# Performance work log

Measured on AMD Instinct MI355X. Metric: run time of the kernel, lower is better.

## Reference

```python
import jax, jax.numpy as jnp
import numpy as np

NUM_BINS = 256
EPS = 1e-8


def setup_inputs() -> dict:
    key = jax.random.key(0)
    k1, k2 = jax.random.split(key)
    x = jax.random.uniform(k1, (4096, 8192), dtype=jnp.float32)
    y = jax.random.uniform(k2, (4096, 8192), dtype=jnp.float32)
    return {"x": x, "y": y}


def reference(x, y):
    # min-max normalize to [0, 1]
    xn = (x - jnp.min(x)) / (jnp.max(x) - jnp.min(x) + EPS)
    yn = (y - jnp.min(y)) / (jnp.max(y) - jnp.min(y) + EPS)
    # bin indices, clamped to [0, NUM_BINS-1] (floor(1.0*N) == N gets clipped)
    x_idx = jnp.clip(jnp.floor(xn * NUM_BINS).astype(jnp.int32), 0, NUM_BINS - 1)
    y_idx = jnp.clip(jnp.floor(yn * NUM_BINS).astype(jnp.int32), 0, NUM_BINS - 1)
    n = x.shape[0] * x.shape[1]
    # joint histogram via scatter-add on flattened (x_idx, y_idx) pairs
    flat = (x_idx * NUM_BINS + y_idx).reshape(-1)
    hist_xy = jnp.zeros((NUM_BINS * NUM_BINS,), jnp.float32).at[flat].add(1.0)
    hist_xy = hist_xy.reshape(NUM_BINS, NUM_BINS)
    p_xy = hist_xy / n
    p_x = jnp.sum(p_xy, axis=1)  # marginal over y
    p_y = jnp.sum(p_xy, axis=0)  # marginal over x
    # MI: sum over cells where p_xy>0 and both marginals>0
    px_py = p_x[:, None] * p_y[None, :]
    valid = (p_xy > 0) & (p_x[:, None] > 0) & (p_y[None, :] > 0)
    safe_pxy = jnp.where(valid, p_xy, 1.0)
    safe_den = jnp.where(valid, px_py, 1.0)
    mi = jnp.sum(jnp.where(valid, p_xy * jnp.log(safe_pxy / safe_den), 0.0))
    # normalized MI
    h_x = -jnp.sum(p_x * jnp.log(p_x + EPS))
    h_y = -jnp.sum(p_y * jnp.log(p_y + EPS))
    mi = mi / (jnp.sqrt(h_x * h_y) + EPS)
    return -mi
```

## Files before the change

kernel.cpp:

```cpp
#include <hip/hip_runtime.h>
#include <stdint.h>
#include <math.h>

#define HIST_BINS   65536
#define HIST_WORDS8 16384
#define NTHR_HIST   1024

__device__ __forceinline__ uint32_t f2key(float f){
    uint32_t u = __float_as_uint(f);
    return (u & 0x80000000u) ? ~u : (u | 0x80000000u);
}
__device__ __forceinline__ float key2f(uint32_t k){
    uint32_t u = (k & 0x80000000u) ? (k ^ 0x80000000u) : ~k;
    return __uint_as_float(u);
}


__global__ void init_mm_kernel(uint32_t* __restrict__ mm){
    mm[0] = 0xFFFFFFFFu;
    mm[1] = 0u;
    mm[2] = 0xFFFFFFFFu;
    mm[3] = 0u;
}

__device__ __forceinline__ void mm4(float4 a, float& mn, float& mx){
    mn = fminf(mn, fminf(fminf(a.x, a.y), fminf(a.z, a.w)));
    mx = fmaxf(mx, fmaxf(fmaxf(a.x, a.y), fmaxf(a.z, a.w)));
}

__global__ void __launch_bounds__(1024)
minmax_kernel(const float4* __restrict__ x, const float4* __restrict__ y,
              uint32_t* __restrict__ mm, int n4, int nblk_per){
    int isy = (blockIdx.x >= (unsigned)nblk_per) ? 1 : 0;
    const float4* __restrict__ src = isy ? y : x;
    int bid = blockIdx.x - isy * nblk_per;
    float mn = INFINITY, mx = -INFINITY;
    int stride = nblk_per * blockDim.x;
    int i = bid * blockDim.x + threadIdx.x;
    for (; i + 7 * stride < n4; i += 8 * stride){
        float4 v0 = src[i];
        float4 v1 = src[i +     stride];
        float4 v2 = src[i + 2 * stride];
        float4 v3 = src[i + 3 * stride];
        float4 v4 = src[i + 4 * stride];
        float4 v5 = src[i + 5 * stride];
        float4 v6 = src[i + 6 * stride];
        float4 v7 = src[i + 7 * stride];
        mm4(v0, mn, mx); mm4(v1, mn, mx); mm4(v2, mn, mx); mm4(v3, mn, mx);
        mm4(v4, mn, mx); mm4(v5, mn, mx); mm4(v6, mn, mx); mm4(v7, mn, mx);
    }
    for (; i < n4; i += stride) mm4(src[i], mn, mx);

    #pragma unroll
    for (int off = 32; off > 0; off >>= 1){
        mn = fminf(mn, __shfl_down(mn, off, 64));
        mx = fmaxf(mx, __shfl_down(mx, off, 64));
    }
    __shared__ float smn[16], smx[16];
    int lane = threadIdx.x & 63, wid = threadIdx.x >> 6;
    if (lane == 0){ smn[wid] = mn; smx[wid] = mx; }
    __syncthreads();
    if (threadIdx.x == 0){
        int nw = blockDim.x >> 6;
        for (int w = 1; w < nw; ++w){
            mn = fminf(mn, smn[w]); mx = fmaxf(mx, smx[w]);
        }
        atomicMin(&mm[isy * 2 + 0], f2key(mn));
        atomicMax(&mm[isy * 2 + 1], f2key(mx));
    }
}

__device__ __forceinline__ void bin_pair(float vx, float vy,
                                         float mnx, float sx, float mny, float sy,
                                         uint32_t* lh){
    int ix = (int)floorf((vx - mnx) * sx);
    int iy = (int)floorf((vy - mny) * sy);
    ix = ix < 0 ? 0 : (ix > 255 ? 255 : ix);
    iy = iy < 0 ? 0 : (iy > 255 ? 255 : iy);
    uint32_t bin = ((uint32_t)ix << 8) | (uint32_t)iy;
    atomicAdd(&lh[bin >> 2], 1u << ((bin & 3u) * 8u));
}

__device__ __forceinline__ void bin4(float4 a, float4 b,
                                     float mnx, float sx, float mny, float sy,
                                     uint32_t* lh){
    bin_pair(a.x, b.x, mnx, sx, mny, sy, lh);
    bin_pair(a.y, b.y, mnx, sx, mny, sy, lh);
    bin_pair(a.z, b.z, mnx, sx, mny, sy, lh);
    bin_pair(a.w, b.w, mnx, sx, mny, sy, lh);
}

__global__ void __launch_bounds__(NTHR_HIST)
hist_kernel(const float4* __restrict__ x, const float4* __restrict__ y,
            const uint32_t* __restrict__ mm, uint32_t* __restrict__ out32,
            int n4, int atomic_flush){
    __shared__ uint32_t lh[HIST_WORDS8];
    for (int w = threadIdx.x; w < HIST_WORDS8; w += blockDim.x) lh[w] = 0u;
    __syncthreads();

    float mnx = key2f(mm[0]);
    float sx  = 256.0f / ((key2f(mm[1]) - mnx) + 1e-8f);
    float mny = key2f(mm[2]);
    float sy  = 256.0f / ((key2f(mm[3]) - mny) + 1e-8f);

    int stride = gridDim.x * blockDim.x;
    int i = blockIdx.x * blockDim.x + threadIdx.x;
    for (; i + 3 * stride < n4; i += 4 * stride){
        float4 a0 = x[i], a1 = x[i + stride], a2 = x[i + 2*stride], a3 = x[i + 3*stride];
        float4 b0 = y[i], b1 = y[i + stride], b2 = y[i + 2*stride], b3 = y[i + 3*stride];
        bin4(a0, b0, mnx, sx, mny, sy, lh);
        bin4(a1, b1, mnx, sx, mny, sy, lh);
        bin4(a2, b2, mnx, sx, mny, sy, lh);
        bin4(a3, b3, mnx, sx, mny, sy, lh);
    }
    for (; i < n4; i += stride){
        float4 a = x[i], b = y[i];
        bin4(a, b, mnx, sx, mny, sy, lh);
    }
    __syncthreads();

    if (!atomic_flush){
        uint32_t* part = out32 + (size_t)blockIdx.x * HIST_WORDS8;
        for (int w = threadIdx.x; w < HIST_WORDS8; w += blockDim.x) part[w] = lh[w];
    } else {
        for (int w = threadIdx.x; w < HIST_WORDS8; w += blockDim.x){
            uint32_t v = lh[w];
            if (v){
                uint32_t c0 = v & 255u, c1 = (v >> 8) & 255u, c2 = (v >> 16) & 255u, c3 = v >> 24;
                if (c0) atomicAdd(&out32[4*w + 0], c0);
                if (c1) atomicAdd(&out32[4*w + 1], c1);
                if (c2) atomicAdd(&out32[4*w + 2], c2);
                if (c3) atomicAdd(&out32[4*w + 3], c3);
            }
        }
    }
}

__global__ void __launch_bounds__(1024)
reduce_kernel(const uint32_t* __restrict__ partials, uint32_t* __restrict__ hist,
              int nparts){
    __shared__ uint32_t sm[64][16][16];
    int t = threadIdx.x;
    int ql = t & 15, g = t >> 4;
    int per = nparts >> 6;
    uint32_t c[16];
    #pragma unroll
    for (int k = 0; k < 16; ++k) c[k] = 0;
    const uint4* base = (const uint4*)partials;
    size_t qoff = (size_t)blockIdx.x * 16 + ql;
    #pragma unroll 8
    for (int j = 0; j < per; ++j){
        uint4 v = base[(size_t)(g * per + j) * (HIST_WORDS8 / 4) + qoff];
        c[ 0] += v.x & 255u; c[ 1] += (v.x >> 8) & 255u; c[ 2] += (v.x >> 16) & 255u; c[ 3] += v.x >> 24;
        c[ 4] += v.y & 255u; c[ 5] += (v.y >> 8) & 255u; c[ 6] += (v.y >> 16) & 255u; c[ 7] += v.y >> 24;
        c[ 8] += v.z & 255u; c[ 9] += (v.z >> 8) & 255u; c[10] += (v.z >> 16) & 255u; c[11] += v.z >> 24;
        c[12] += v.w & 255u; c[13] += (v.w >> 8) & 255u; c[14] += (v.w >> 16) & 255u; c[15] += v.w >> 24;
    }
    #pragma unroll
    for (int k = 0; k < 16; ++k) sm[g][k][ql] = c[k];
    __syncthreads();
    if (t < 256){
        int q2 = t & 15;
        int k  = t >> 4;
        uint32_t s = 0;
        #pragma unroll 8
        for (int gg = 0; gg < 64; ++gg) s += sm[gg][k][q2];
        hist[((size_t)blockIdx.x * 16 + q2) * 16 + k] = s;
    }
}

__device__ double bsum1024(double v, double* red, int t){
    #pragma unroll
    for (int off = 32; off > 0; off >>= 1) v += __shfl_down(v, off, 64);
    __syncthreads();
    if ((t & 63) == 0) red[t >> 6] = v;
    __syncthreads();
    if (t == 0){
        double s = 0.0;
        for (int w = 0; w < 16; ++w) s += red[w];
        v = s;
    }
    return v;
}

__global__ void __launch_bounds__(1024)
finalize_kernel(const uint32_t* __restrict__ hist, float* __restrict__ out, int n){
    __shared__ uint32_t rsum[256];
    __shared__ uint32_t csum4[4][256];
    __shared__ uint32_t csum[256];
    __shared__ double red[16];
    int t = threadIdx.x;

    {
        int r = t >> 2, q = t & 3;
        const uint4* hp = (const uint4*)(hist + r * 256 + q * 64);
        uint32_t s = 0;
        #pragma unroll
        for (int k = 0; k < 16; ++k){
            uint4 v = hp[k];
            s += v.x + v.y + v.z + v.w;
        }
        s += __shfl_down(s, 2, 64);
        s += __shfl_down(s, 1, 64);
        if (q == 0) rsum[r] = s;
    }
    {
        int c = t & 255, g = t >> 8;
        const uint32_t* hp = hist + g * 64 * 256 + c;
        uint32_t s = 0;
        #pragma unroll 8
        for (int r = 0; r < 64; ++r) s += hp[r * 256];
        csum4[g][c] = s;
    }
    __syncthreads();
    if (t < 256) csum[t] = csum4[0][t] + csum4[1][t] + csum4[2][t] + csum4[3][t];
    __syncthreads();

    const double invn = 1.0 / (double)n;
    const double dn = (double)n;

    double mi = 0.0;
    {
        int c = t & 255, rb = t >> 8;
        double cs = (double)csum[c];
        for (int k = 0; k < 64; ++k){
            int r = k * 4 + rb;
            uint32_t cnt = hist[r * 256 + c];
            if (cnt){
                double rs = (double)rsum[r];
                double ratio = ((double)cnt * dn) / (rs * cs);
                mi += (double)cnt * (double)logf((float)ratio);
            }
        }
        mi *= invn;
    }
    double hx = 0.0, hy = 0.0;
    if (t < 256){
        double px = (double)rsum[t] * invn;
        double py = (double)csum[t] * invn;
        hx = px * log(px + 1e-8);
        hy = py * log(py + 1e-8);
    }
    double mi_s = bsum1024(mi, red, t);
    double hx_s = bsum1024(hx, red, t);
    double hy_s = bsum1024(hy, red, t);
    if (t == 0){
        double h_x = -hx_s, h_y = -hy_s;
        double nmi = mi_s / (sqrt(h_x * h_y) + 1e-8);
        out[0] = (float)(-nmi);
    }
}

extern "C" void kernel_launch(void* const* d_in, const int* in_sizes, int n_in,
                              void* d_out, int out_size, void* d_ws, size_t ws_size,
                              hipStream_t stream){
    const float* x = (const float*)d_in[0];
    const float* y = (const float*)d_in[1];
    float* out = (float*)d_out;
    uint32_t* ws = (uint32_t*)d_ws;
    uint32_t* hist = ws;
    uint32_t* mm = ws + HIST_BINS;
    uint32_t* partials = ws + HIST_BINS + 64;

    int n  = in_sizes[0];
    int n4 = n / 4;

    size_t need512 = ((size_t)HIST_BINS + 64 + (size_t)512 * HIST_WORDS8) * 4;
    size_t need256 = ((size_t)HIST_BINS + 64 + (size_t)256 * HIST_WORDS8) * 4;
    int nblk, atomic_flush;
    if (ws_size >= need512)      { nblk = 512; atomic_flush = 0; }
    else if (ws_size >= need256) { nblk = 256; atomic_flush = 0; }
    else                         { nblk = 512; atomic_flush = 1; }

    if (atomic_flush)
        hipMemsetAsync(hist, 0, HIST_BINS * sizeof(uint32_t), stream);
    init_mm_kernel<<<1, 1, 0, stream>>>(mm);
    minmax_kernel<<<512, 1024, 0, stream>>>((const float4*)x, (const float4*)y, mm, n4, 256);
    hist_kernel<<<nblk, NTHR_HIST, 0, stream>>>((const float4*)x, (const float4*)y, mm,
                                                atomic_flush ? hist : partials, n4, atomic_flush);
    if (!atomic_flush)
        reduce_kernel<<<256, 1024, 0, stream>>>(partials, hist, nblk);
    finalize_kernel<<<1, 1024, 0, stream>>>(hist, out, n);
}
```

Before: 367.9 us.

## Use contiguous per-block segments, nontemporal loads, and fuse marginals into reduce

Minmax and histogram kernels now have each block walk its own contiguous segment instead of a grid-stride pattern, and the histogram kernel reads inputs with nontemporal loads. The reduce kernel now also computes row sums and column sums of the joint histogram, using atomics for the column sums. Finalize can then skip recomputing the marginals and reads the histogram in a vectorized row-major order. The goal is better DRAM locality and less serial work in the single-block finalize, at the cost of extra atomics and an init kernel that clears the column-sum buffer.

```diff
diff --git a/kernel.cpp b/kernel.cpp
--- a/kernel.cpp
+++ b/kernel.cpp
@@ -4,7 +4,10 @@
 
 #define HIST_BINS   65536
 #define HIST_WORDS8 16384
-#define NTHR_HIST   1024
+
+typedef float f4 __attribute__((ext_vector_type(4)));
+
+__device__ __forceinline__ f4 ldnt(const f4* p){ return __builtin_nontemporal_load(p); }
 
 __device__ __forceinline__ uint32_t f2key(float f){
     uint32_t u = __float_as_uint(f);
@@ -16,55 +19,50 @@
 }
 
 
-__global__ void init_mm_kernel(uint32_t* __restrict__ mm){
-    mm[0] = 0xFFFFFFFFu;
-    mm[1] = 0u;
-    mm[2] = 0xFFFFFFFFu;
-    mm[3] = 0u;
-}
-
-__device__ __forceinline__ void mm4(float4 a, float& mn, float& mx){
-    mn = fminf(mn, fminf(fminf(a.x, a.y), fminf(a.z, a.w)));
-    mx = fmaxf(mx, fmaxf(fmaxf(a.x, a.y), fmaxf(a.z, a.w)));
+__global__ void init_kernel(uint32_t* __restrict__ mm, uint32_t* __restrict__ csum){
+    int t = threadIdx.x;
+    if (t < 4) mm[t] = (t & 1) ? 0u : 0xFFFFFFFFu;
+    csum[t] = 0u;
+}
+
+__device__ __forceinline__ void mm4(f4 a, float& mn, float& mx){
+    mn = fminf(mn, fminf(fminf(a[0], a[1]), fminf(a[2], a[3])));
+    mx = fmaxf(mx, fmaxf(fmaxf(a[0], a[1]), fmaxf(a[2], a[3])));
 }
 
 __global__ void __launch_bounds__(1024)
-minmax_kernel(const float4* __restrict__ x, const float4* __restrict__ y,
+minmax_kernel(const f4* __restrict__ x, const f4* __restrict__ y,
               uint32_t* __restrict__ mm, int n4, int nblk_per){
     int isy = (blockIdx.x >= (unsigned)nblk_per) ? 1 : 0;
-    const float4* __restrict__ src = isy ? y : x;
+    const f4* __restrict__ src = isy ? y : x;
     int bid = blockIdx.x - isy * nblk_per;
+    int seg = n4 / nblk_per;
+    int base = bid * seg;
+    const int chunk = 1024 * 8;
     float mn = INFINITY, mx = -INFINITY;
-    int stride = nblk_per * blockDim.x;
-    int i = bid * blockDim.x + threadIdx.x;
-    for (; i + 7 * stride < n4; i += 8 * stride){
-        float4 v0 = src[i];
-        float4 v1 = src[i +     stride];
-        float4 v2 = src[i + 2 * stride];
-        float4 v3 = src[i + 3 * stride];
-        float4 v4 = src[i + 4 * stride];
-        float4 v5 = src[i + 5 * stride];
-        float4 v6 = src[i + 6 * stride];
-        float4 v7 = src[i + 7 * stride];
+    int off = 0;
+    for (; off + chunk <= seg; off += chunk){
+        const f4* p = src + base + off + threadIdx.x;
+        f4 v0 = p[0],        v1 = p[1024],     v2 = p[2 * 1024], v3 = p[3 * 1024];
+        f4 v4 = p[4 * 1024], v5 = p[5 * 1024], v6 = p[6 * 1024], v7 = p[7 * 1024];
         mm4(v0, mn, mx); mm4(v1, mn, mx); mm4(v2, mn, mx); mm4(v3, mn, mx);
         mm4(v4, mn, mx); mm4(v5, mn, mx); mm4(v6, mn, mx); mm4(v7, mn, mx);
     }
-    for (; i < n4; i += stride) mm4(src[i], mn, mx);
+    for (int i = base + off + threadIdx.x; i < base + seg; i += 1024) mm4(src[i], mn, mx);
+    if (bid == nblk_per - 1)
+        for (int i = nblk_per * seg + threadIdx.x; i < n4; i += 1024) mm4(src[i], mn, mx);
 
     #pragma unroll
-    for (int off = 32; off > 0; off >>= 1){
-        mn = fminf(mn, __shfl_down(mn, off, 64));
-        mx = fmaxf(mx, __shfl_down(mx, off, 64));
+    for (int o = 32; o > 0; o >>= 1){
+        mn = fminf(mn, __shfl_down(mn, o, 64));
+        mx = fmaxf(mx, __shfl_down(mx, o, 64));
     }
     __shared__ float smn[16], smx[16];
     int lane = threadIdx.x & 63, wid = threadIdx.x >> 6;
     if (lane == 0){ smn[wid] = mn; smx[wid] = mx; }
     __syncthreads();
     if (threadIdx.x == 0){
-        int nw = blockDim.x >> 6;
-        for (int w = 1; w < nw; ++w){
-            mn = fminf(mn, smn[w]); mx = fmaxf(mx, smx[w]);
-        }
+        for (int w = 1; w < 16; ++w){ mn = fminf(mn, smn[w]); mx = fmaxf(mx, smx[w]); }
         atomicMin(&mm[isy * 2 + 0], f2key(mn));
         atomicMax(&mm[isy * 2 + 1], f2key(mx));
     }
@@ -81,17 +79,17 @@
     atomicAdd(&lh[bin >> 2], 1u << ((bin & 3u) * 8u));
 }
 
-__device__ __forceinline__ void bin4(float4 a, float4 b,
+__device__ __forceinline__ void bin4(f4 a, f4 b,
                                      float mnx, float sx, float mny, float sy,
                                      uint32_t* lh){
-    bin_pair(a.x, b.x, mnx, sx, mny, sy, lh);
-    bin_pair(a.y, b.y, mnx, sx, mny, sy, lh);
-    bin_pair(a.z, b.z, mnx, sx, mny, sy, lh);
-    bin_pair(a.w, b.w, mnx, sx, mny, sy, lh);
-}
-
-__global__ void __launch_bounds__(NTHR_HIST)
-hist_kernel(const float4* __restrict__ x, const float4* __restrict__ y,
+    bin_pair(a[0], b[0], mnx, sx, mny, sy, lh);
+    bin_pair(a[1], b[1], mnx, sx, mny, sy, lh);
+    bin_pair(a[2], b[2], mnx, sx, mny, sy, lh);
+    bin_pair(a[3], b[3], mnx, sx, mny, sy, lh);
+}
+
+__global__ void __launch_bounds__(1024)
+hist_kernel(const f4* __restrict__ x, const f4* __restrict__ y,
             const uint32_t* __restrict__ mm, uint32_t* __restrict__ out32,
             int n4, int atomic_flush){
     __shared__ uint32_t lh[HIST_WORDS8];
@@ -103,20 +101,27 @@
     float mny = key2f(mm[2]);
     float sy  = 256.0f / ((key2f(mm[3]) - mny) + 1e-8f);
 
-    int stride = gridDim.x * blockDim.x;
-    int i = blockIdx.x * blockDim.x + threadIdx.x;
-    for (; i + 3 * stride < n4; i += 4 * stride){
-        float4 a0 = x[i], a1 = x[i + stride], a2 = x[i + 2*stride], a3 = x[i + 3*stride];
-        float4 b0 = y[i], b1 = y[i + stride], b2 = y[i + 2*stride], b3 = y[i + 3*stride];
+    int seg  = n4 / gridDim.x;
+    int base = blockIdx.x * seg;
+    const int chunk = 1024 * 4;
+    int off = 0;
+    for (; off + chunk <= seg; off += chunk){
+        const f4* px = x + base + off + threadIdx.x;
+        const f4* py = y + base + off + threadIdx.x;
+        f4 a0 = ldnt(px),            a1 = ldnt(px + 1024);
+        f4 a2 = ldnt(px + 2 * 1024), a3 = ldnt(px + 3 * 1024);
+        f4 b0 = ldnt(py),            b1 = ldnt(py + 1024);
+        f4 b2 = ldnt(py + 2 * 1024), b3 = ldnt(py + 3 * 1024);
         bin4(a0, b0, mnx, sx, mny, sy, lh);
         bin4(a1, b1, mnx, sx, mny, sy, lh);
         bin4(a2, b2, mnx, sx, mny, sy, lh);
         bin4(a3, b3, mnx, sx, mny, sy, lh);
     }
-    for (; i < n4; i += stride){
-        float4 a = x[i], b = y[i];
-        bin4(a, b, mnx, sx, mny, sy, lh);
-    }
+    for (int i = base + off + threadIdx.x; i < base + seg; i += 1024)
+        bin4(x[i], y[i], mnx, sx, mny, sy, lh);
+    if (blockIdx.x == gridDim.x - 1)
+        for (int i = gridDim.x * seg + threadIdx.x; i < n4; i += 1024)
+            bin4(x[i], y[i], mnx, sx, mny, sy, lh);
     __syncthreads();
 
     if (!atomic_flush){
@@ -138,7 +143,7 @@
 
 __global__ void __launch_bounds__(1024)
 reduce_kernel(const uint32_t* __restrict__ partials, uint32_t* __restrict__ hist,
-              int nparts){
+              uint32_t* __restrict__ rsum, uint32_t* __restrict__ csum, int nparts){
     __shared__ uint32_t sm[64][16][16];
     int t = threadIdx.x;
     int ql = t & 15, g = t >> 4;
@@ -159,19 +164,30 @@
     #pragma unroll
     for (int k = 0; k < 16; ++k) sm[g][k][ql] = c[k];
     __syncthreads();
+    uint32_t s = 0;
     if (t < 256){
         int q2 = t & 15;
         int k  = t >> 4;
-        uint32_t s = 0;
         #pragma unroll 8
         for (int gg = 0; gg < 64; ++gg) s += sm[gg][k][q2];
-        hist[((size_t)blockIdx.x * 16 + q2) * 16 + k] = s;
-    }
+        hist[(size_t)blockIdx.x * 256 + q2 * 16 + k] = s;
+        atomicAdd(&csum[q2 * 16 + k], s);
+    }
+    __syncthreads();
+    uint32_t* flat = &sm[0][0][0];
+    if (t < 256){
+        uint32_t bs = s;
+        #pragma unroll
+        for (int o = 32; o > 0; o >>= 1) bs += __shfl_down(bs, o, 64);
+        if ((t & 63) == 0) flat[t >> 6] = bs;
+    }
+    __syncthreads();
+    if (t == 0) rsum[blockIdx.x] = flat[0] + flat[1] + flat[2] + flat[3];
 }
 
 __device__ double bsum1024(double v, double* red, int t){
     #pragma unroll
-    for (int off = 32; off > 0; off >>= 1) v += __shfl_down(v, off, 64);
+    for (int o = 32; o > 0; o >>= 1) v += __shfl_down(v, o, 64);
     __syncthreads();
     if ((t & 63) == 0) red[t >> 6] = v;
     __syncthreads();
@@ -184,36 +200,38 @@
 }
 
 __global__ void __launch_bounds__(1024)
-finalize_kernel(const uint32_t* __restrict__ hist, float* __restrict__ out, int n){
-    __shared__ uint32_t rsum[256];
+finalize_kernel(const uint32_t* __restrict__ hist,
+                const uint32_t* __restrict__ rsum, const uint32_t* __restrict__ csum,
+                float* __restrict__ out, int n, int marg){
+    __shared__ uint32_t lrs[256], lcs[256];
     __shared__ uint32_t csum4[4][256];
-    __shared__ uint32_t csum[256];
     __shared__ double red[16];
     int t = threadIdx.x;
 
-    {
-        int r = t >> 2, q = t & 3;
-        const uint4* hp = (const uint4*)(hist + r * 256 + q * 64);
-        uint32_t s = 0;
-        #pragma unroll
-        for (int k = 0; k < 16; ++k){
-            uint4 v = hp[k];
-            s += v.x + v.y + v.z + v.w;
+    if (!marg){
+        if (t < 256){ lrs[t] = rsum[t]; lcs[t] = csum[t]; }
+    } else {
+        {
+            int r = t >> 2, q = t & 3;
+            const uint4* hp = (const uint4*)(hist + r * 256 + q * 64);
+            uint32_t s = 0;
+            #pragma unroll
+            for (int k = 0; k < 16; ++k){ uint4 v = hp[k]; s += v.x + v.y + v.z + v.w; }
+            s += __shfl_down(s, 2, 64);
+            s += __shfl_down(s, 1, 64);
+            if (q == 0) lrs[r] = s;
         }
-        s += __shfl_down(s, 2, 64);
-        s += __shfl_down(s, 1, 64);
-        if (q == 0) rsum[r] = s;
-    }
-    {
-        int c = t & 255, g = t >> 8;
-        const uint32_t* hp = hist + g * 64 * 256 + c;
-        uint32_t s = 0;
-        #pragma unroll 8
-        for (int r = 0; r < 64; ++r) s += hp[r * 256];
-        csum4[g][c] = s;
-    }
-    __syncthreads();
-    if (t < 256) csum[t] = csum4[0][t] + csum4[1][t] + csum4[2][t] + csum4[3][t];
+        {
+            int c = t & 255, g = t >> 8;
+            const uint32_t* hp = hist + g * 64 * 256 + c;
+            uint32_t s = 0;
+            #pragma unroll 8
+            for (int r = 0; r < 64; ++r) s += hp[r * 256];
+            csum4[g][c] = s;
+        }
+        __syncthreads();
+        if (t < 256) lcs[t] = csum4[0][t] + csum4[1][t] + csum4[2][t] + csum4[3][t];
+    }
     __syncthreads();
 
     const double invn = 1.0 / (double)n;
@@ -221,23 +239,27 @@
 
     double mi = 0.0;
     {
-        int c = t & 255, rb = t >> 8;
-        double cs = (double)csum[c];
-        for (int k = 0; k < 64; ++k){
-            int r = k * 4 + rb;
-            uint32_t cnt = hist[r * 256 + c];
-            if (cnt){
-                double rs = (double)rsum[r];
-                double ratio = ((double)cnt * dn) / (rs * cs);
-                mi += (double)cnt * (double)logf((float)ratio);
+        int q = t & 63, g = t >> 6;
+        const uint4* h4 = (const uint4*)hist;
+        for (int k = 0; k < 16; ++k){
+            int r = g * 16 + k;
+            uint4 v = h4[r * 64 + q];
+            double rs = (double)lrs[r];
+            uint32_t cc[4] = {v.x, v.y, v.z, v.w};
+            #pragma unroll
+            for (int j = 0; j < 4; ++j){
+                if (cc[j]){
+                    double ratio = ((double)cc[j] * dn) / (rs * (double)lcs[q * 4 + j]);
+                    mi += (double)cc[j] * (double)logf((float)ratio);
+                }
             }
         }
         mi *= invn;
     }
     double hx = 0.0, hy = 0.0;
     if (t < 256){
-        double px = (double)rsum[t] * invn;
-        double py = (double)csum[t] * invn;
+        double px = (double)lrs[t] * invn;
+        double py = (double)lcs[t] * invn;
         hx = px * log(px + 1e-8);
         hy = py * log(py + 1e-8);
     }
@@ -254,19 +276,22 @@
 extern "C" void kernel_launch(void* const* d_in, const int* in_sizes, int n_in,
                               void* d_out, int out_size, void* d_ws, size_t ws_size,
                               hipStream_t stream){
-    const float* x = (const float*)d_in[0];
-    const float* y = (const float*)d_in[1];
+    const f4* x = (const f4*)d_in[0];
+    const f4* y = (const f4*)d_in[1];
     float* out = (float*)d_out;
     uint32_t* ws = (uint32_t*)d_ws;
     uint32_t* hist = ws;
-    uint32_t* mm = ws + HIST_BINS;
-    uint32_t* partials = ws + HIST_BINS + 64;
+    uint32_t* mm   = ws + HIST_BINS;
+    uint32_t* rsum = ws + HIST_BINS + 64;
+    uint32_t* csum = ws + HIST_BINS + 64 + 256;
+    uint32_t* partials = ws + HIST_BINS + 64 + 512;
 
     int n  = in_sizes[0];
     int n4 = n / 4;
 
-    size_t need512 = ((size_t)HIST_BINS + 64 + (size_t)512 * HIST_WORDS8) * 4;
-    size_t need256 = ((size_t)HIST_BINS + 64 + (size_t)256 * HIST_WORDS8) * 4;
+    size_t head = (size_t)HIST_BINS + 64 + 512;
+    size_t need512 = (head + (size_t)512 * HIST_WORDS8) * 4;
+    size_t need256 = (head + (size_t)256 * HIST_WORDS8) * 4;
     int nblk, atomic_flush;
     if (ws_size >= need512)      { nblk = 512; atomic_flush = 0; }
     else if (ws_size >= need256) { nblk = 256; atomic_flush = 0; }
@@ -274,11 +299,11 @@
 
     if (atomic_flush)
         hipMemsetAsync(hist, 0, HIST_BINS * sizeof(uint32_t), stream);
-    init_mm_kernel<<<1, 1, 0, stream>>>(mm);
-    minmax_kernel<<<512, 1024, 0, stream>>>((const float4*)x, (const float4*)y, mm, n4, 256);
-    hist_kernel<<<nblk, NTHR_HIST, 0, stream>>>((const float4*)x, (const float4*)y, mm,
-                                                atomic_flush ? hist : partials, n4, atomic_flush);
+    init_kernel<<<1, 256, 0, stream>>>(mm, csum);
+    minmax_kernel<<<512, 1024, 0, stream>>>(x, y, mm, n4, 256);
+    hist_kernel<<<nblk, 1024, 0, stream>>>(x, y, mm,
+                                           atomic_flush ? hist : partials, n4, atomic_flush);
     if (!atomic_flush)
-        reduce_kernel<<<256, 1024, 0, stream>>>(partials, hist, nblk);
-    finalize_kernel<<<1, 1024, 0, stream>>>(hist, out, n);
-}
+        reduce_kernel<<<256, 1024, 0, stream>>>(partials, hist, rsum, csum, nblk);
+    finalize_kernel<<<1, 1024, 0, stream>>>(hist, rsum, csum, out, n, atomic_flush);
+}
```

After: 371.3 us. No clear change (+0.9%).
